# Kernel optimization log

Measured on AMD Instinct MI355X. Metric: run time of the kernel, lower is better.

The kernel has to match this reference:

```python
import jax, jax.numpy as jnp
import numpy as np

HEADS = 4
DIM_HEAD = 32
EPS = 1e-5


def setup_inputs() -> dict:
    key = jax.random.key(0)
    ks = jax.random.split(key, 3)
    b, c, h, w = 32, 256, 64, 64
    hidden = HEADS * DIM_HEAD  # 128
    x = jax.random.normal(ks[0], (b, c, h, w), dtype=jnp.float32)
    w_qkv = jax.random.normal(ks[1], (3 * hidden, c), dtype=jnp.float32) * 0.02
    w_out = jax.random.normal(ks[2], (c, hidden), dtype=jnp.float32) * 0.02
    b_out = jnp.zeros((c,), dtype=jnp.float32)
    gn_w = jnp.ones((c,), dtype=jnp.float32)
    gn_b = jnp.zeros((c,), dtype=jnp.float32)
    return {"x": x, "w_qkv": w_qkv, "w_out": w_out, "b_out": b_out,
            "gn_w": gn_w, "gn_b": gn_b}


def reference(x, w_qkv, w_out, b_out, gn_w, gn_b):
    b, c, h, w = x.shape
    n = h * w
    scale = DIM_HEAD ** (-0.5)
    # 1x1 conv (no bias) -> qkv, shape (b, 3*hidden, h, w)
    qkv = jnp.einsum('bchw,oc->bohw', x, w_qkv)
    qkv = qkv.reshape(b, 3, HEADS, DIM_HEAD, n)
    q, k, v = qkv[:, 0], qkv[:, 1], qkv[:, 2]  # each (b, H, d, n)
    q = jax.nn.softmax(q, axis=-2) * scale     # softmax over d
    k = jax.nn.softmax(k, axis=-1)             # softmax over n
    # linear attention core
    context = jnp.einsum('bhdn,bhen->bhde', k, v)   # (b, H, d, e)
    out = jnp.einsum('bhde,bhdn->bhen', context, q)  # (b, H, e, n)
    out = out.reshape(b, HEADS * DIM_HEAD, h, w)
    # 1x1 conv with bias
    out = jnp.einsum('bchw,oc->bohw', out, w_out) + b_out[None, :, None, None]
    # GroupNorm(1, dim): normalize over (C, H, W) per sample
    mean = out.mean(axis=(1, 2, 3), keepdims=True)
    var = out.var(axis=(1, 2, 3), keepdims=True)
    out = (out - mean) * jax.lax.rsqrt(var + EPS)
    out = out * gn_w[None, :, None, None] + gn_b[None, :, None, None]
    return out
```

## Files before the change

### kernel.cpp

```cpp
#include <hip/hip_runtime.h>
#include <math.h>

#define B_ 32
#define C_ 256
#define N_ 4096
#define HID_ 128
#define OC3_ 384
#define HEADS_ 4
#define DH_ 32
#define LNM_ (C_*N_)
#define CTXP_ 4

typedef unsigned short u16;
typedef __attribute__((ext_vector_type(8))) short short8;
typedef __attribute__((ext_vector_type(4))) float f32x4;

__device__ inline u16 f2b(float f) {
  union { float f; unsigned int u; } c; c.f = f;
  unsigned int u = c.u;
  return (u16)((u + 0x7fffu + ((u >> 16) & 1u)) >> 16);
}
__device__ inline float b2f(u16 b) {
  union { float f; unsigned int u; } c; c.u = (unsigned int)b << 16; return c.f;
}
__device__ inline unsigned int cvt_pk(float lo, float hi) {
  unsigned int r;
  asm("v_cvt_pk_bf16_f32 %0, %1, %2" : "=v"(r) : "v"(lo), "v"(hi));
  return r;
}
__device__ inline void load_lds16(const u16* g, u16* l) {
  __builtin_amdgcn_global_load_lds(
      (const __attribute__((address_space(1))) void*)g,
      (__attribute__((address_space(3))) void*)l, 16, 0, 0);
}

template<int KDIM, bool OUTBF16, bool BFUSED>
__global__ __launch_bounds__(256) void k_gemm_mfma(
    const float* __restrict__ Af, const u16* __restrict__ Ball,
    const float* __restrict__ Xall, void* __restrict__ Call,
    const float* __restrict__ bias, float* __restrict__ bsum, int Mtot) {
  int b = blockIdx.z;
  int m0 = blockIdx.y * 128, n0 = blockIdx.x * 128;
  __shared__ __align__(16) u16 As[4096];
  __shared__ __align__(16) u16 Bs[4096];
  __shared__ float red[8];
  int tid = threadIdx.x;
  int w = tid >> 6, l = tid & 63, l16 = l & 15, quad = l >> 4;
  int wm = w & 1, wn = w >> 1;
  f32x4 acc[4][4] = {};

  const u16* Bt = BFUSED ? nullptr : (Ball + (size_t)b * N_ * KDIM);
  const float* Xb = BFUSED ? (Xall + (size_t)b * KDIM * N_) : nullptr;

  for (int k0 = 0; k0 < KDIM; k0 += 32) {
    {
      int m = tid & 127, kh = tid >> 7;
      const float* ga = Af + (size_t)(m0 + m) * KDIM + k0 + kh * 16;
      float4 v0 = *(const float4*)(ga + 0);
      float4 v1 = *(const float4*)(ga + 4);
      float4 v2 = *(const float4*)(ga + 8);
      float4 v3 = *(const float4*)(ga + 12);
      uint4 q0, q1;
      q0.x = cvt_pk(v0.x, v0.y); q0.y = cvt_pk(v0.z, v0.w);
      q0.z = cvt_pk(v1.x, v1.y); q0.w = cvt_pk(v1.z, v1.w);
      q1.x = cvt_pk(v2.x, v2.y); q1.y = cvt_pk(v2.z, v2.w);
      q1.z = cvt_pk(v3.x, v3.y); q1.w = cvt_pk(v3.z, v3.w);
      *(uint4*)&As[(size_t)(kh * 2 + 0) * 1024 + m * 8] = q0;
      *(uint4*)&As[(size_t)(kh * 2 + 1) * 1024 + m * 8] = q1;
    }
    if constexpr (BFUSED) {
      int nl = (tid & 63) * 2, cb = tid >> 6;
      const float* gb = Xb + (size_t)(k0 + cb * 8) * N_ + n0 + nl;
      float2 e[8];
      #pragma unroll
      for (int ci = 0; ci < 8; ci++) e[ci] = *(const float2*)(gb + (size_t)ci * N_);
      uint4 lo, hi;
      lo.x = cvt_pk(e[0].x, e[1].x); lo.y = cvt_pk(e[2].x, e[3].x);
      lo.z = cvt_pk(e[4].x, e[5].x); lo.w = cvt_pk(e[6].x, e[7].x);
      hi.x = cvt_pk(e[0].y, e[1].y); hi.y = cvt_pk(e[2].y, e[3].y);
      hi.z = cvt_pk(e[4].y, e[5].y); hi.w = cvt_pk(e[6].y, e[7].y);
      int prow = nl >> 1;
      *(uint4*)&Bs[(size_t)cb * 1024 + (size_t)prow * 8] = lo;
      *(uint4*)&Bs[(size_t)cb * 1024 + (size_t)(64 + prow) * 8] = hi;
    } else {
      #pragma unroll
      for (int i = 0; i < 2; i++) {
        int chunk = i * 256 + tid;
        int c = chunk >> 7, m = chunk & 127;
        const u16* gb = Bt + (size_t)(n0 + m) * KDIM + k0 + c * 8;
        u16* lb = Bs + (size_t)(i * 256 + (tid & ~63)) * 8;
        load_lds16(gb, lb);
      }
    }
    __syncthreads();
    short8 af[4], bf[4];
    #pragma unroll
    for (int mi = 0; mi < 4; mi++)
      af[mi] = *(const short8*)&As[(size_t)(quad * 128 + wm * 64 + mi * 16 + l16) * 8];
    #pragma unroll
    for (int nj = 0; nj < 4; nj++) {
      int rr = wn * 64 + nj * 16 + l16;
      int pp;
      if constexpr (BFUSED) pp = (rr >> 1) | ((rr & 1) << 6);
      else pp = rr;
      bf[nj] = *(const short8*)&Bs[(size_t)(quad * 128 + pp) * 8];
    }
    #pragma unroll
    for (int mi = 0; mi < 4; mi++)
      #pragma unroll
      for (int nj = 0; nj < 4; nj++)
        acc[mi][nj] = __builtin_amdgcn_mfma_f32_16x16x32_bf16(af[mi], bf[nj], acc[mi][nj], 0, 0, 0);
    __syncthreads();
  }

  if constexpr (OUTBF16) {
    u16* Co = (u16*)Call + (size_t)b * Mtot * N_;
    u16* lw = As + w * 1024;
    #pragma unroll
    for (int mi = 0; mi < 4; mi++) {
      #pragma unroll
      for (int nj = 0; nj < 4; nj++)
        #pragma unroll
        for (int r = 0; r < 4; r++)
          lw[(quad * 4 + r) * 64 + nj * 16 + l16] = f2b(acc[mi][nj][r]);
      #pragma unroll
      for (int p = 0; p < 2; p++) {
        int chunk = p * 64 + l;
        int row = chunk >> 3, cc = chunk & 7;
        uint4 v = *(const uint4*)&lw[chunk * 8];
        *(uint4*)&Co[(size_t)(m0 + wm * 64 + mi * 16 + row) * N_ + n0 + wn * 64 + cc * 8] = v;
      }
    }
  } else {
    float* Co = (float*)Call + (size_t)b * Mtot * N_;
    float s1 = 0.f, s2 = 0.f;
    #pragma unroll
    for (int mi = 0; mi < 4; mi++)
      #pragma unroll
      for (int r = 0; r < 4; r++) {
        int m = m0 + wm * 64 + mi * 16 + quad * 4 + r;
        float bv = bias[m];
        #pragma unroll
        for (int nj = 0; nj < 4; nj++) {
          int n = n0 + wn * 64 + nj * 16 + l16;
          float v = acc[mi][nj][r] + bv;
          s1 += v; s2 += v * v;
          Co[(size_t)m * N_ + n] = v;
        }
      }
    #pragma unroll
    for (int o = 32; o; o >>= 1) { s1 += __shfl_xor(s1, o); s2 += __shfl_xor(s2, o); }
    if (l == 0) { red[w] = s1; red[4 + w] = s2; }
    __syncthreads();
    if (tid == 0) {
      atomicAdd(&bsum[2 * b],     red[0] + red[1] + red[2] + red[3]);
      atomicAdd(&bsum[2 * b + 1], red[4] + red[5] + red[6] + red[7]);
    }
  }
}

__global__ __launch_bounds__(256) void k_kstats(const u16* __restrict__ qkvb,
    float* __restrict__ rmax, float* __restrict__ rinv, float* __restrict__ bsum) {
  int r = blockIdx.x;
  int b = r >> 7, rem = r & 127;
  const u16* row = qkvb + (size_t)b * OC3_ * N_ + (size_t)(HID_ + rem) * N_;
  int tid = threadIdx.x;
  if (r == 0 && tid < 64) bsum[tid] = 0.f;
  float v[16];
  #pragma unroll
  for (int p = 0; p < 2; p++) {
    uint4 u = *(const uint4*)&row[(size_t)(p * 256 + tid) * 8];
    unsigned int uu[4] = {u.x, u.y, u.z, u.w};
    #pragma unroll
    for (int j = 0; j < 4; j++) {
      v[p * 8 + j * 2 + 0] = b2f((u16)(uu[j] & 0xffff));
      v[p * 8 + j * 2 + 1] = b2f((u16)(uu[j] >> 16));
    }
  }
  float m = -1e30f;
  #pragma unroll
  for (int i = 0; i < 16; i++) m = fmaxf(m, v[i]);
  #pragma unroll
  for (int o = 32; o; o >>= 1) m = fmaxf(m, __shfl_xor(m, o));
  __shared__ float sm[4], ss[4];
  int w = tid >> 6;
  if ((tid & 63) == 0) sm[w] = m;
  __syncthreads();
  m = fmaxf(fmaxf(sm[0], sm[1]), fmaxf(sm[2], sm[3]));
  float s = 0.f;
  #pragma unroll
  for (int i = 0; i < 16; i++) s += __expf(v[i] - m);
  #pragma unroll
  for (int o = 32; o; o >>= 1) s += __shfl_xor(s, o);
  if ((tid & 63) == 0) ss[w] = s;
  __syncthreads();
  if (tid == 0) {
    rmax[r] = m;
    rinv[r] = 1.f / (ss[0] + ss[1] + ss[2] + ss[3]);
  }
}

__global__ __launch_bounds__(256) void k_context(const u16* __restrict__ qkvb,
    const float* __restrict__ rmax, const float* __restrict__ rinv,
    float* __restrict__ ctxp) {
  int blk = blockIdx.x, bh = blockIdx.y;
  int b = bh >> 2, hd = bh & 3;
  const u16* kb = qkvb + (size_t)b * OC3_ * N_ + (size_t)(HID_ + hd * DH_) * N_;
  const u16* vb = qkvb + (size_t)b * OC3_ * N_ + (size_t)(2 * HID_ + hd * DH_) * N_;
  __shared__ float redl[4096];
  int tid = threadIdx.x;
  int w = tid >> 6, l = tid & 63, l16 = l & 15, quad = l >> 4;
  float rm[2], ri[2];
  #pragma unroll
  for (int mi = 0; mi < 2; mi++) {
    rm[mi] = rmax[bh * 32 + mi * 16 + l16];
    ri[mi] = rinv[bh * 32 + mi * 16 + l16];
  }
  f32x4 acc[2][2] = {};
  int nbase = blk * 1024 + w * 256 + quad * 8;
  #pragma unroll
  for (int kk = 0; kk < 8; kk++) {
    int n0 = nbase + kk * 32;
    short8 af[2], bf[2];
    #pragma unroll
    for (int nj = 0; nj < 2; nj++)
      bf[nj] = *(const short8*)&vb[(size_t)(nj * 16 + l16) * N_ + n0];
    #pragma unroll
    for (int mi = 0; mi < 2; mi++) {
      uint4 u = *(const uint4*)&kb[(size_t)(mi * 16 + l16) * N_ + n0];
      unsigned int uu[4] = {u.x, u.y, u.z, u.w};
      union { unsigned int u[4]; short8 s; } pk;
      #pragma unroll
      for (int j = 0; j < 4; j++) {
        float lo = __expf(b2f((u16)(uu[j] & 0xffff)) - rm[mi]) * ri[mi];
        float hi = __expf(b2f((u16)(uu[j] >> 16))     - rm[mi]) * ri[mi];
        pk.u[j] = cvt_pk(lo, hi);
      }
      af[mi] = pk.s;
    }
    #pragma unroll
    for (int mi = 0; mi < 2; mi++)
      #pragma unroll
      for (int nj = 0; nj < 2; nj++)
        acc[mi][nj] = __builtin_amdgcn_mfma_f32_16x16x32_bf16(af[mi], bf[nj], acc[mi][nj], 0, 0, 0);
  }
  #pragma unroll
  for (int mi = 0; mi < 2; mi++)
    #pragma unroll
    for (int nj = 0; nj < 2; nj++)
      #pragma unroll
      for (int r = 0; r < 4; r++)
        redl[w * 1024 + (mi * 16 + quad * 4 + r) * 32 + nj * 16 + l16] = acc[mi][nj][r];
  __syncthreads();
  float* cp = ctxp + (size_t)blk * 131072 + (size_t)bh * 1024;
  #pragma unroll
  for (int j = 0; j < 4; j++) {
    int idx = j * 256 + tid;
    cp[idx] = redl[idx] + redl[1024 + idx] + redl[2048 + idx] + redl[3072 + idx];
  }
}

__global__ __launch_bounds__(256) void k_attnout(const u16* __restrict__ qkvb,
    const float* __restrict__ ctxp, u16* __restrict__ hidt) {
  int tile = blockIdx.x, bh = blockIdx.y;
  int b = bh >> 2, hd = bh & 3;
  const u16* qbase = qkvb + (size_t)b * OC3_ * N_ + (size_t)(hd * DH_) * N_;
  __shared__ float cs[32][40];
  __shared__ unsigned int hs[256][16];
  int tid = threadIdx.x;
  for (int idx = tid; idx < 1024; idx += 256) {
    float s = 0.f;
    #pragma unroll
    for (int p = 0; p < CTXP_; p++)
      s += ctxp[(size_t)p * 131072 + (size_t)bh * 1024 + idx];
    int d = idx >> 5, e = idx & 31;
    cs[d][e] = s;
  }
  __syncthreads();
  int n = tile * 256 + tid;
  float q[32];
  float m = -1e30f;
  #pragma unroll
  for (int d = 0; d < 32; d++) { q[d] = b2f(qbase[(size_t)d * N_ + n]); m = fmaxf(m, q[d]); }
  float s = 0.f;
  #pragma unroll
  for (int d = 0; d < 32; d++) { q[d] = __expf(q[d] - m); s += q[d]; }
  float inv = 0.17677669529663687f / s;
  #pragma unroll
  for (int d = 0; d < 32; d++) q[d] *= inv;
  #pragma unroll
  for (int e0 = 0; e0 < 32; e0 += 4) {
    f32x4 a = {};
    #pragma unroll
    for (int d = 0; d < 32; d++) {
      f32x4 c4 = *(const f32x4*)&cs[d][e0];
      a += q[d] * c4;
    }
    hs[tid][e0 / 2 + 0] = cvt_pk(a[0], a[1]);
    hs[tid][e0 / 2 + 1] = cvt_pk(a[2], a[3]);
  }
  __syncthreads();
  #pragma unroll
  for (int it = 0; it < 8; it++) {
    int q2 = it * 256 + tid;
    int nl = q2 >> 3, c2 = q2 & 7;
    uint2 v = *(const uint2*)&hs[nl][c2 * 2];
    *(uint2*)&hidt[((size_t)b * N_ + tile * 256 + nl) * HID_ + hd * 32 + c2 * 4] = v;
  }
}

__global__ void k_finalize(float* __restrict__ bsum) {
  int b = threadIdx.x;
  if (b < B_) {
    float s1 = bsum[2 * b], s2 = bsum[2 * b + 1];
    float mean = s1 * (1.f / LNM_);
    float var = s2 * (1.f / LNM_) - mean * mean;
    bsum[2 * b] = mean;
    bsum[2 * b + 1] = rsqrtf(var + 1e-5f);
  }
}

__global__ __launch_bounds__(256) void k_norm(float* __restrict__ out,
    const float* __restrict__ bsum, const float* __restrict__ gnw,
    const float* __restrict__ gnb) {
  size_t v = (size_t)blockIdx.x * 256 + threadIdx.x;
  int c = (int)((v >> 10) & 255);
  int b = (int)(v >> 18);
  float mean = bsum[2 * b], rstd = bsum[2 * b + 1];
  float w = gnw[c] * rstd;
  float sh = gnb[c] - mean * w;
  float4 x = ((const float4*)out)[v];
  x.x = x.x * w + sh; x.y = x.y * w + sh;
  x.z = x.z * w + sh; x.w = x.w * w + sh;
  ((float4*)out)[v] = x;
}

extern "C" void kernel_launch(void* const* d_in, const int* in_sizes, int n_in,
                              void* d_out, int out_size, void* d_ws, size_t ws_size,
                              hipStream_t stream) {
  const float* x     = (const float*)d_in[0];
  const float* w_qkv = (const float*)d_in[1];
  const float* w_out = (const float*)d_in[2];
  const float* b_out = (const float*)d_in[3];
  const float* gn_w  = (const float*)d_in[4];
  const float* gn_b  = (const float*)d_in[5];
  float* out = (float*)d_out;

  u16* qkvb = (u16*)d_ws;
  u16* hidt = qkvb + (size_t)B_ * OC3_ * N_;
  float* ctx  = (float*)(hidt + (size_t)B_ * N_ * HID_);
  float* bsum = ctx + CTXP_ * 131072;
  float* rmax = bsum + 64;
  float* rinv = rmax + 4096;

  k_gemm_mfma<256, true, true><<<dim3(32, 3, 32), 256, 0, stream>>>(
      w_qkv, nullptr, x, qkvb, nullptr, nullptr, OC3_);
  k_kstats<<<4096, 256, 0, stream>>>(qkvb, rmax, rinv, bsum);
  k_context<<<dim3(CTXP_, 128), 256, 0, stream>>>(qkvb, rmax, rinv, ctx);
  k_attnout<<<dim3(16, 128), 256, 0, stream>>>(qkvb, ctx, hidt);
  k_gemm_mfma<128, false, false><<<dim3(32, 2, 32), 256, 0, stream>>>(
      w_out, hidt, nullptr, out, b_out, bsum, C_);
  k_finalize<<<1, 64, 0, stream>>>(bsum);
  k_norm<<<32768, 256, 0, stream>>>(out, bsum, gn_w, gn_b);
}
```

Before: 419.0 us.

## Double-buffer LDS tiles and prefetch next K-slices into registers in MFMA GEMM

Restructures the GEMM K-loop into a software pipeline with two LDS buffers for the A and B tiles. Global loads for tile t+2 are issued into registers and tile t+1 is written into the alternate LDS buffer while tile t is computed. This leaves one barrier per iteration instead of two and is meant to hide global memory latency behind MFMA work. In exchange it doubles LDS use and raises register pressure, which could lower occupancy.

Result: no change. 427.2 us (+1.9%).

```diff
diff --git a/kernel.cpp b/kernel.cpp
--- a/kernel.cpp
+++ b/kernel.cpp
@@ -39,10 +39,11 @@
     const float* __restrict__ Af, const u16* __restrict__ Ball,
     const float* __restrict__ Xall, void* __restrict__ Call,
     const float* __restrict__ bias, float* __restrict__ bsum, int Mtot) {
+  constexpr int NT = KDIM / 32;
   int b = blockIdx.z;
   int m0 = blockIdx.y * 128, n0 = blockIdx.x * 128;
-  __shared__ __align__(16) u16 As[4096];
-  __shared__ __align__(16) u16 Bs[4096];
+  __shared__ __align__(16) u16 As[2][4096];
+  __shared__ __align__(16) u16 Bs[2][4096];
   __shared__ float red[8];
   int tid = threadIdx.x;
   int w = tid >> 6, l = tid & 63, l16 = l & 15, quad = l >> 4;
@@ -52,70 +53,106 @@
   const u16* Bt = BFUSED ? nullptr : (Ball + (size_t)b * N_ * KDIM);
   const float* Xb = BFUSED ? (Xall + (size_t)b * KDIM * N_) : nullptr;
 
-  for (int k0 = 0; k0 < KDIM; k0 += 32) {
-    {
-      int m = tid & 127, kh = tid >> 7;
-      const float* ga = Af + (size_t)(m0 + m) * KDIM + k0 + kh * 16;
-      float4 v0 = *(const float4*)(ga + 0);
-      float4 v1 = *(const float4*)(ga + 4);
-      float4 v2 = *(const float4*)(ga + 8);
-      float4 v3 = *(const float4*)(ga + 12);
-      uint4 q0, q1;
-      q0.x = cvt_pk(v0.x, v0.y); q0.y = cvt_pk(v0.z, v0.w);
-      q0.z = cvt_pk(v1.x, v1.y); q0.w = cvt_pk(v1.z, v1.w);
-      q1.x = cvt_pk(v2.x, v2.y); q1.y = cvt_pk(v2.z, v2.w);
-      q1.z = cvt_pk(v3.x, v3.y); q1.w = cvt_pk(v3.z, v3.w);
-      *(uint4*)&As[(size_t)(kh * 2 + 0) * 1024 + m * 8] = q0;
-      *(uint4*)&As[(size_t)(kh * 2 + 1) * 1024 + m * 8] = q1;
-    }
-    if constexpr (BFUSED) {
-      int nl = (tid & 63) * 2, cb = tid >> 6;
-      const float* gb = Xb + (size_t)(k0 + cb * 8) * N_ + n0 + nl;
-      float2 e[8];
-      #pragma unroll
-      for (int ci = 0; ci < 8; ci++) e[ci] = *(const float2*)(gb + (size_t)ci * N_);
-      uint4 lo, hi;
-      lo.x = cvt_pk(e[0].x, e[1].x); lo.y = cvt_pk(e[2].x, e[3].x);
-      lo.z = cvt_pk(e[4].x, e[5].x); lo.w = cvt_pk(e[6].x, e[7].x);
-      hi.x = cvt_pk(e[0].y, e[1].y); hi.y = cvt_pk(e[2].y, e[3].y);
-      hi.z = cvt_pk(e[4].y, e[5].y); hi.w = cvt_pk(e[6].y, e[7].y);
-      int prow = nl >> 1;
-      *(uint4*)&Bs[(size_t)cb * 1024 + (size_t)prow * 8] = lo;
-      *(uint4*)&Bs[(size_t)cb * 1024 + (size_t)(64 + prow) * 8] = hi;
-    } else {
-      #pragma unroll
-      for (int i = 0; i < 2; i++) {
-        int chunk = i * 256 + tid;
-        int c = chunk >> 7, m = chunk & 127;
-        const u16* gb = Bt + (size_t)(n0 + m) * KDIM + k0 + c * 8;
-        u16* lb = Bs + (size_t)(i * 256 + (tid & ~63)) * 8;
-        load_lds16(gb, lb);
-      }
-    }
-    __syncthreads();
+  int am = tid & 127, akh = tid >> 7;
+  const float* gaBase = Af + (size_t)(m0 + am) * KDIM + akh * 16;
+  float4 a0, a1, a2, a3;
+  int nl = (tid & 63) * 2, cb = tid >> 6;
+  float2 e0, e1, e2, e3, e4, e5, e6, e7;
+
+  auto a_load = [&](int k0) {
+    const float* ga = gaBase + k0;
+    a0 = *(const float4*)(ga + 0);
+    a1 = *(const float4*)(ga + 4);
+    a2 = *(const float4*)(ga + 8);
+    a3 = *(const float4*)(ga + 12);
+  };
+  auto a_write = [&](int bufi) {
+    uint4 q0, q1;
+    q0.x = cvt_pk(a0.x, a0.y); q0.y = cvt_pk(a0.z, a0.w);
+    q0.z = cvt_pk(a1.x, a1.y); q0.w = cvt_pk(a1.z, a1.w);
+    q1.x = cvt_pk(a2.x, a2.y); q1.y = cvt_pk(a2.z, a2.w);
+    q1.z = cvt_pk(a3.x, a3.y); q1.w = cvt_pk(a3.z, a3.w);
+    *(uint4*)&As[bufi][(size_t)(akh * 2 + 0) * 1024 + am * 8] = q0;
+    *(uint4*)&As[bufi][(size_t)(akh * 2 + 1) * 1024 + am * 8] = q1;
+  };
+  auto b_load = [&](int k0) {
+    const float* gb = Xb + (size_t)(k0 + cb * 8) * N_ + n0 + nl;
+    e0 = *(const float2*)(gb + 0 * (size_t)N_);
+    e1 = *(const float2*)(gb + 1 * (size_t)N_);
+    e2 = *(const float2*)(gb + 2 * (size_t)N_);
+    e3 = *(const float2*)(gb + 3 * (size_t)N_);
+    e4 = *(const float2*)(gb + 4 * (size_t)N_);
+    e5 = *(const float2*)(gb + 5 * (size_t)N_);
+    e6 = *(const float2*)(gb + 6 * (size_t)N_);
+    e7 = *(const float2*)(gb + 7 * (size_t)N_);
+  };
+  auto b_write = [&](int bufi) {
+    uint4 lo, hi;
+    lo.x = cvt_pk(e0.x, e1.x); lo.y = cvt_pk(e2.x, e3.x);
+    lo.z = cvt_pk(e4.x, e5.x); lo.w = cvt_pk(e6.x, e7.x);
+    hi.x = cvt_pk(e0.y, e1.y); hi.y = cvt_pk(e2.y, e3.y);
+    hi.z = cvt_pk(e4.y, e5.y); hi.w = cvt_pk(e6.y, e7.y);
+    int prow = nl >> 1;
+    *(uint4*)&Bs[bufi][(size_t)cb * 1024 + (size_t)prow * 8] = lo;
+    *(uint4*)&Bs[bufi][(size_t)cb * 1024 + (size_t)(64 + prow) * 8] = hi;
+  };
+  auto b_async = [&](int k0, int bufi) {
+    #pragma unroll
+    for (int i = 0; i < 2; i++) {
+      int chunk = i * 256 + tid;
+      int c = chunk >> 7, m = chunk & 127;
+      const u16* gb = Bt + (size_t)(n0 + m) * KDIM + k0 + c * 8;
+      u16* lb = &Bs[bufi][(size_t)(i * 256 + (tid & ~63)) * 8];
+      load_lds16(gb, lb);
+    }
+  };
+  auto compute = [&](int bufi) {
     short8 af[4], bf[4];
     #pragma unroll
     for (int mi = 0; mi < 4; mi++)
-      af[mi] = *(const short8*)&As[(size_t)(quad * 128 + wm * 64 + mi * 16 + l16) * 8];
+      af[mi] = *(const short8*)&As[bufi][(size_t)(quad * 128 + wm * 64 + mi * 16 + l16) * 8];
     #pragma unroll
     for (int nj = 0; nj < 4; nj++) {
       int rr = wn * 64 + nj * 16 + l16;
       int pp;
       if constexpr (BFUSED) pp = (rr >> 1) | ((rr & 1) << 6);
       else pp = rr;
-      bf[nj] = *(const short8*)&Bs[(size_t)(quad * 128 + pp) * 8];
+      bf[nj] = *(const short8*)&Bs[bufi][(size_t)(quad * 128 + pp) * 8];
     }
     #pragma unroll
     for (int mi = 0; mi < 4; mi++)
       #pragma unroll
       for (int nj = 0; nj < 4; nj++)
         acc[mi][nj] = __builtin_amdgcn_mfma_f32_16x16x32_bf16(af[mi], bf[nj], acc[mi][nj], 0, 0, 0);
+  };
+
+  a_load(0);
+  if constexpr (BFUSED) b_load(0); else b_async(0, 0);
+  a_write(0);
+  if constexpr (BFUSED) b_write(0);
+  a_load(32);
+  if constexpr (BFUSED) b_load(32);
+  __syncthreads();
+
+  #pragma unroll
+  for (int t = 0; t < NT; t++) {
+    int cur = t & 1, nxt = cur ^ 1;
+    if (t + 1 < NT) {
+      a_write(nxt);
+      if constexpr (BFUSED) b_write(nxt);
+      else b_async((t + 1) * 32, nxt);
+      if (t + 2 < NT) {
+        a_load((t + 2) * 32);
+        if constexpr (BFUSED) b_load((t + 2) * 32);
+      }
+    }
+    compute(cur);
     __syncthreads();
   }
 
   if constexpr (OUTBF16) {
     u16* Co = (u16*)Call + (size_t)b * Mtot * N_;
-    u16* lw = As + w * 1024;
+    u16* lw = &As[0][w * 1024];
     #pragma unroll
     for (int mi = 0; mi < 4; mi++) {
       #pragma unroll
```

## Precast weights to bf16 and prefetch next X tile in GEMM loop

Applied to the files above, without the earlier changes.

Adds a small kernel that converts both weight matrices to bf16 once per call and zeroes the norm accumulators, so the GEMMs can stream A tiles straight into LDS with async global-to-LDS loads instead of loading fp32 and converting every tile. The fused QKV GEMM now register-prefetches the next X tile while MFMAs run on the current one, a form of software pipelining. The cost is one extra kernel launch, more live registers from the prefetched float2 values, and more workspace for the bf16 weights.

New measurement: 408.2 us. 2.6% less time.

```diff
diff --git a/kernel.cpp b/kernel.cpp
--- a/kernel.cpp
+++ b/kernel.cpp
@@ -34,11 +34,21 @@
       (__attribute__((address_space(3))) void*)l, 16, 0, 0);
 }
 
+__global__ void k_cast_w(const float* __restrict__ wq, const float* __restrict__ wo,
+                         u16* __restrict__ wqb, u16* __restrict__ wob,
+                         float* __restrict__ bsum) {
+  int i = blockIdx.x * 256 + threadIdx.x;
+  if (i < OC3_ * C_) wqb[i] = f2b(wq[i]);
+  if (i < C_ * HID_) wob[i] = f2b(wo[i]);
+  if (i < 64) bsum[i] = 0.f;
+}
+
 template<int KDIM, bool OUTBF16, bool BFUSED>
 __global__ __launch_bounds__(256) void k_gemm_mfma(
-    const float* __restrict__ Af, const u16* __restrict__ Ball,
+    const u16* __restrict__ A, const u16* __restrict__ Ball,
     const float* __restrict__ Xall, void* __restrict__ Call,
     const float* __restrict__ bias, float* __restrict__ bsum, int Mtot) {
+  constexpr int NT = KDIM / 32;
   int b = blockIdx.z;
   int m0 = blockIdx.y * 128, n0 = blockIdx.x * 128;
   __shared__ __align__(16) u16 As[4096];
@@ -52,47 +62,51 @@
   const u16* Bt = BFUSED ? nullptr : (Ball + (size_t)b * N_ * KDIM);
   const float* Xb = BFUSED ? (Xall + (size_t)b * KDIM * N_) : nullptr;
 
-  for (int k0 = 0; k0 < KDIM; k0 += 32) {
-    {
-      int m = tid & 127, kh = tid >> 7;
-      const float* ga = Af + (size_t)(m0 + m) * KDIM + k0 + kh * 16;
-      float4 v0 = *(const float4*)(ga + 0);
-      float4 v1 = *(const float4*)(ga + 4);
-      float4 v2 = *(const float4*)(ga + 8);
-      float4 v3 = *(const float4*)(ga + 12);
-      uint4 q0, q1;
-      q0.x = cvt_pk(v0.x, v0.y); q0.y = cvt_pk(v0.z, v0.w);
-      q0.z = cvt_pk(v1.x, v1.y); q0.w = cvt_pk(v1.z, v1.w);
-      q1.x = cvt_pk(v2.x, v2.y); q1.y = cvt_pk(v2.z, v2.w);
-      q1.z = cvt_pk(v3.x, v3.y); q1.w = cvt_pk(v3.z, v3.w);
-      *(uint4*)&As[(size_t)(kh * 2 + 0) * 1024 + m * 8] = q0;
-      *(uint4*)&As[(size_t)(kh * 2 + 1) * 1024 + m * 8] = q1;
-    }
-    if constexpr (BFUSED) {
-      int nl = (tid & 63) * 2, cb = tid >> 6;
-      const float* gb = Xb + (size_t)(k0 + cb * 8) * N_ + n0 + nl;
-      float2 e[8];
-      #pragma unroll
-      for (int ci = 0; ci < 8; ci++) e[ci] = *(const float2*)(gb + (size_t)ci * N_);
-      uint4 lo, hi;
-      lo.x = cvt_pk(e[0].x, e[1].x); lo.y = cvt_pk(e[2].x, e[3].x);
-      lo.z = cvt_pk(e[4].x, e[5].x); lo.w = cvt_pk(e[6].x, e[7].x);
-      hi.x = cvt_pk(e[0].y, e[1].y); hi.y = cvt_pk(e[2].y, e[3].y);
-      hi.z = cvt_pk(e[4].y, e[5].y); hi.w = cvt_pk(e[6].y, e[7].y);
-      int prow = nl >> 1;
-      *(uint4*)&Bs[(size_t)cb * 1024 + (size_t)prow * 8] = lo;
-      *(uint4*)&Bs[(size_t)cb * 1024 + (size_t)(64 + prow) * 8] = hi;
-    } else {
-      #pragma unroll
-      for (int i = 0; i < 2; i++) {
-        int chunk = i * 256 + tid;
-        int c = chunk >> 7, m = chunk & 127;
-        const u16* gb = Bt + (size_t)(n0 + m) * KDIM + k0 + c * 8;
-        u16* lb = Bs + (size_t)(i * 256 + (tid & ~63)) * 8;
-        load_lds16(gb, lb);
-      }
-    }
-    __syncthreads();
+  int nl = (tid & 63) * 2, cb = tid >> 6;
+  float2 e0, e1, e2, e3, e4, e5, e6, e7;
+
+  auto a_async = [&](int k0) {
+    #pragma unroll
+    for (int i = 0; i < 2; i++) {
+      int chunk = i * 256 + tid;
+      int c = chunk >> 7, m = chunk & 127;
+      const u16* ga = A + (size_t)(m0 + m) * KDIM + k0 + c * 8;
+      u16* la = As + (size_t)(i * 256 + (tid & ~63)) * 8;
+      load_lds16(ga, la);
+    }
+  };
+  auto b_async = [&](int k0) {
+    #pragma unroll
+    for (int i = 0; i < 2; i++) {
+      int chunk = i * 256 + tid;
+      int c = chunk >> 7, m = chunk & 127;
+      const u16* gb = Bt + (size_t)(n0 + m) * KDIM + k0 + c * 8;
+      u16* lb = Bs + (size_t)(i * 256 + (tid & ~63)) * 8;
+      load_lds16(gb, lb);
+    }
+  };
+  auto b_load = [&](int k0) {
+    const float* gb = Xb + (size_t)(k0 + cb * 8) * N_ + n0 + nl;
+    e0 = *(const float2*)(gb + 0 * (size_t)N_);
+    e1 = *(const float2*)(gb + 1 * (size_t)N_);
+    e2 = *(const float2*)(gb + 2 * (size_t)N_);
+    e3 = *(const float2*)(gb + 3 * (size_t)N_);
+    e4 = *(const float2*)(gb + 4 * (size_t)N_);
+    e5 = *(const float2*)(gb + 5 * (size_t)N_);
+    e6 = *(const float2*)(gb + 6 * (size_t)N_);
+    e7 = *(const float2*)(gb + 7 * (size_t)N_);
+  };
+  auto b_write = [&]() {
+    uint4 lo, hi;
+    lo.x = cvt_pk(e0.x, e1.x); lo.y = cvt_pk(e2.x, e3.x);
+    lo.z = cvt_pk(e4.x, e5.x); lo.w = cvt_pk(e6.x, e7.x);
+    hi.x = cvt_pk(e0.y, e1.y); hi.y = cvt_pk(e2.y, e3.y);
+    hi.z = cvt_pk(e4.y, e5.y); hi.w = cvt_pk(e6.y, e7.y);
+    int prow = nl >> 1;
+    *(uint4*)&Bs[(size_t)cb * 1024 + (size_t)prow * 8] = lo;
+    *(uint4*)&Bs[(size_t)cb * 1024 + (size_t)(64 + prow) * 8] = hi;
+  };
+  auto compute = [&]() {
     short8 af[4], bf[4];
     #pragma unroll
     for (int mi = 0; mi < 4; mi++)
@@ -110,6 +124,19 @@
       #pragma unroll
       for (int nj = 0; nj < 4; nj++)
         acc[mi][nj] = __builtin_amdgcn_mfma_f32_16x16x32_bf16(af[mi], bf[nj], acc[mi][nj], 0, 0, 0);
+  };
+
+  if constexpr (BFUSED) b_load(0);
+  #pragma unroll
+  for (int t = 0; t < NT; t++) {
+    if constexpr (BFUSED) b_write();
+    a_async(t * 32);
+    if constexpr (!BFUSED) b_async(t * 32);
+    __syncthreads();
+    if constexpr (BFUSED) {
+      if (t + 1 < NT) b_load((t + 1) * 32);
+    }
+    compute();
     __syncthreads();
   }
 
@@ -160,12 +187,11 @@
 }
 
 __global__ __launch_bounds__(256) void k_kstats(const u16* __restrict__ qkvb,
-    float* __restrict__ rmax, float* __restrict__ rinv, float* __restrict__ bsum) {
+    float* __restrict__ rmax, float* __restrict__ rinv) {
   int r = blockIdx.x;
   int b = r >> 7, rem = r & 127;
   const u16* row = qkvb + (size_t)b * OC3_ * N_ + (size_t)(HID_ + rem) * N_;
   int tid = threadIdx.x;
-  if (r == 0 && tid < 64) bsum[tid] = 0.f;
   float v[16];
   #pragma unroll
   for (int p = 0; p < 2; p++) {
@@ -352,14 +378,17 @@
   float* bsum = ctx + CTXP_ * 131072;
   float* rmax = bsum + 64;
   float* rinv = rmax + 4096;
-
+  u16* wqb = (u16*)(rinv + 4096);
+  u16* wob = wqb + OC3_ * C_;
+
+  k_cast_w<<<384, 256, 0, stream>>>(w_qkv, w_out, wqb, wob, bsum);
   k_gemm_mfma<256, true, true><<<dim3(32, 3, 32), 256, 0, stream>>>(
-      w_qkv, nullptr, x, qkvb, nullptr, nullptr, OC3_);
-  k_kstats<<<4096, 256, 0, stream>>>(qkvb, rmax, rinv, bsum);
+      wqb, nullptr, x, qkvb, nullptr, nullptr, OC3_);
+  k_kstats<<<4096, 256, 0, stream>>>(qkvb, rmax, rinv);
   k_context<<<dim3(CTXP_, 128), 256, 0, stream>>>(qkvb, rmax, rinv, ctx);
   k_attnout<<<dim3(16, 128), 256, 0, stream>>>(qkvb, ctx, hidt);
   k_gemm_mfma<128, false, false><<<dim3(32, 2, 32), 256, 0, stream>>>(
-      w_out, hidt, nullptr, out, b_out, bsum, C_);
+      wob, hidt, nullptr, out, b_out, bsum, C_);
   k_finalize<<<1, 64, 0, stream>>>(bsum);
   k_norm<<<32768, 256, 0, stream>>>(out, bsum, gn_w, gn_b);
 }
```
